# Kernel tuning notes

Measured on AMD Instinct MI355X. Metric: run time of the kernel, lower is better.

## Reference

```python
import jax, jax.numpy as jnp
import numpy as np
from jax import lax

DT = 0.1
B, T, SD, CD, H = 1024, 200, 64, 32, 512


def setup_inputs() -> dict:
    key = jax.random.key(0)
    k0, k1, k2, k3 = jax.random.split(key, 4)
    scale1 = 1.0 / np.sqrt(SD + CD)
    scale2 = 1.0 / np.sqrt(H)
    return {
        "x0": jax.random.normal(k0, (B, SD), dtype=jnp.float32),
        "controls": jax.random.normal(k1, (B, T, CD), dtype=jnp.float32),
        "W1": jax.random.normal(k2, (SD + CD, H), dtype=jnp.float32) * scale1,
        "b1": jnp.zeros((H,), dtype=jnp.float32),
        "W2": jax.random.normal(k3, (H, SD), dtype=jnp.float32) * scale2,
        "b2": jnp.zeros((SD,), dtype=jnp.float32),
    }


def reference(x0, controls, W1, b1, W2, b2):
    # dynamics: x_{t+1} = x + dt * MLP(concat(x, u)); rollout with true data dependency
    def step(x, u):
        h = jnp.tanh(jnp.concatenate([x, u], axis=-1) @ W1 + b1)  # [B, H]
        x_next = x + DT * (h @ W2 + b2)                           # [B, SD]
        return x_next, x_next

    controls_t = jnp.swapaxes(controls, 0, 1)  # [T, B, CD]
    _, xs = lax.scan(step, x0, controls_t)     # xs: [T, B, SD]
    states = jnp.concatenate([x0[:, None, :], jnp.swapaxes(xs, 0, 1)], axis=1)  # [B, T+1, SD]
    return states
```

## Files before the change

kernel.cpp:

```cpp
#include <hip/hip_runtime.h>
#include <cstddef>


constexpr int B_  = 1024;
constexpr int T_  = 200;
constexpr int SD_ = 64;
constexpr int CD_ = 32;
constexpr int H_  = 512;
constexpr int KD_ = SD_ + CD_;
constexpr float DT_ = 0.1f;
constexpr int ROWS_ = 4;
constexpr int THREADS_ = 1024;
constexpr int KHALF_ = 48;
constexpr int CHUNK_ = 32;

__global__ __launch_bounds__(THREADS_)
void rollout_split_kernel(
    const float* __restrict__ x0,
    const float* __restrict__ ctrl,
    const float* __restrict__ W1,
    const float* __restrict__ b1,
    const float* __restrict__ W2,
    const float* __restrict__ b2,
    float* __restrict__ out)
{
    __shared__ float xcT[KD_][ROWS_];
    __shared__ float part1[ROWS_][H_];
    __shared__ float hbuf[ROWS_][H_];
    __shared__ float part2[ROWS_][16][SD_];

    const int tid = threadIdx.x;
    const int r0  = blockIdx.x * ROWS_;

    const int j     = tid & (H_ - 1);
    const int g     = tid >> 9;
    const int kbase = g * KHALF_;
    float w1p[KHALF_];
    #pragma unroll
    for (int i = 0; i < KHALF_; ++i)
        w1p[i] = W1[(size_t)(kbase + i) * H_ + j];

    const int wv = tid >> 6;
    const int sl = tid & 63;
    const int jb = wv * CHUNK_;
    float w2p[CHUNK_];
    #pragma unroll
    for (int i = 0; i < CHUNK_; ++i)
        w2p[i] = W2[(size_t)(jb + i) * SD_ + sl];

    const float bj = b1[j];

    const int rf = (tid >> 6) & 3;
    const int sf = tid & 63;
    const float bs = b2[sf];

    const int  lt = tid - 512;
    const bool loader = (lt >= 0) && (lt < ROWS_ * CD_);
    const int  lr = (lt >> 5) & 3;
    const int  lc = lt & 31;
    const size_t ctrl_base = (size_t)(r0 + lr) * T_ * CD_ + lc;

    if (tid < ROWS_ * SD_) {
        const float v = x0[(size_t)(r0 + rf) * SD_ + sf];
        xcT[sf][rf] = v;
        out[(size_t)(r0 + rf) * (T_ + 1) * SD_ + sf] = v;
    }
    if (loader) xcT[SD_ + lc][lr] = ctrl[ctrl_base];
    __syncthreads();

    for (int t = 0; t < T_; ++t) {
        float cpre = 0.f;
        if (loader && (t + 1 < T_))
            cpre = ctrl[ctrl_base + (size_t)(t + 1) * CD_];

        float a0 = 0.f, a1 = 0.f, a2 = 0.f, a3 = 0.f;
        #pragma unroll
        for (int i = 0; i < KHALF_; ++i) {
            const float4 xv = *(const float4*)&xcT[kbase + i][0];
            const float  w  = w1p[i];
            a0 += xv.x * w;
            a1 += xv.y * w;
            a2 += xv.z * w;
            a3 += xv.w * w;
        }
        if (g == 1) {
            part1[0][j] = a0;  part1[1][j] = a1;
            part1[2][j] = a2;  part1[3][j] = a3;
        }
        __syncthreads();

        if (g == 0) {
            hbuf[0][j] = tanhf(bj + a0 + part1[0][j]);
            hbuf[1][j] = tanhf(bj + a1 + part1[1][j]);
            hbuf[2][j] = tanhf(bj + a2 + part1[2][j]);
            hbuf[3][j] = tanhf(bj + a3 + part1[3][j]);
        } else if (loader && (t + 1 < T_)) {
            xcT[SD_ + lc][lr] = cpre;
        }
        __syncthreads();

        #pragma unroll
        for (int r = 0; r < ROWS_; ++r) {
            float p = 0.f;
            #pragma unroll
            for (int i4 = 0; i4 < CHUNK_; i4 += 4) {
                const float4 hv = *(const float4*)&hbuf[r][jb + i4];
                p += hv.x * w2p[i4]     + hv.y * w2p[i4 + 1]
                   + hv.z * w2p[i4 + 2] + hv.w * w2p[i4 + 3];
            }
            part2[r][wv][sl] = p;
        }
        __syncthreads();

        if (tid < ROWS_ * SD_) {
            float acc = part2[rf][0][sf];
            #pragma unroll
            for (int c = 1; c < 16; ++c) acc += part2[rf][c][sf];
            const float xnew = xcT[sf][rf] + DT_ * (acc + bs);
            xcT[sf][rf] = xnew;
            out[(size_t)(r0 + rf) * (T_ + 1) * SD_ + (size_t)(t + 1) * SD_ + sf] = xnew;
        }
        __syncthreads();
    }
}

extern "C" void kernel_launch(void* const* d_in, const int* in_sizes, int n_in,
                              void* d_out, int out_size, void* d_ws, size_t ws_size,
                              hipStream_t stream) {
    const float* x0   = (const float*)d_in[0];
    const float* ctrl = (const float*)d_in[1];
    const float* W1   = (const float*)d_in[2];
    const float* b1   = (const float*)d_in[3];
    const float* W2   = (const float*)d_in[4];
    const float* b2   = (const float*)d_in[5];
    float* out = (float*)d_out;

    dim3 grid(B_ / ROWS_);
    dim3 block(THREADS_);
    rollout_split_kernel<<<grid, block, 0, stream>>>(x0, ctrl, W1, b1, W2, b2, out);
}
```

Before: 790.5 us.

## Split W1 reduction into four K-slices with packed float2 FMAs

Restructures the first matmul so each thread owns two hidden columns over a quarter of the K dimension, using packed two-wide FMA builtins. A shared-memory reduction over the four slices is then done by all 1024 threads, each computing two tanh values, so every thread does equal work instead of half the block idling during the tanh phase. The second matmul is also rewritten with packed FMAs over all four rows at once. The cost is a larger partial-sum buffer and more shared-memory traffic per step.

```diff
diff --git a/kernel.cpp b/kernel.cpp
--- a/kernel.cpp
+++ b/kernel.cpp
@@ -11,11 +11,14 @@
 constexpr float DT_ = 0.1f;
 constexpr int ROWS_ = 4;
 constexpr int THREADS_ = 1024;
-constexpr int KHALF_ = 48;
+constexpr int KSLICES_ = 4;
+constexpr int KLEN_ = KD_ / KSLICES_;
 constexpr int CHUNK_ = 32;
 
+typedef float f2 __attribute__((ext_vector_type(2)));
+
 __global__ __launch_bounds__(THREADS_)
-void rollout_split_kernel(
+void rollout_r12_kernel(
     const float* __restrict__ x0,
     const float* __restrict__ ctrl,
     const float* __restrict__ W1,
@@ -25,20 +28,21 @@
     float* __restrict__ out)
 {
     __shared__ float xcT[KD_][ROWS_];
-    __shared__ float part1[ROWS_][H_];
-    __shared__ float hbuf[ROWS_][H_];
+    __shared__ float part1[KSLICES_][ROWS_][H_];
+    __shared__ float pbuf[ROWS_][H_];
     __shared__ float part2[ROWS_][16][SD_];
 
     const int tid = threadIdx.x;
     const int r0  = blockIdx.x * ROWS_;
 
-    const int j     = tid & (H_ - 1);
-    const int g     = tid >> 9;
-    const int kbase = g * KHALF_;
-    float w1p[KHALF_];
+    const int jp    = tid & 255;
+    const int ks    = tid >> 8;
+    const int j0    = jp * 2;
+    const int kbase = ks * KLEN_;
+    f2 w1p[KLEN_];
     #pragma unroll
-    for (int i = 0; i < KHALF_; ++i)
-        w1p[i] = W1[(size_t)(kbase + i) * H_ + j];
+    for (int i = 0; i < KLEN_; ++i)
+        w1p[i] = *(const f2*)&W1[(size_t)(kbase + i) * H_ + j0];
 
     const int wv = tid >> 6;
     const int sl = tid & 63;
@@ -48,7 +52,9 @@
     for (int i = 0; i < CHUNK_; ++i)
         w2p[i] = W2[(size_t)(jb + i) * SD_ + sl];
 
-    const float bj = b1[j];
+    const int rF  = tid >> 8;
+    const int jjF = (tid & 255) * 2;
+    const f2 bj2 = {b1[jjF], b1[jjF + 1]};
 
     const int rf = (tid >> 6) & 3;
     const int sf = tid & 63;
@@ -73,42 +79,60 @@
         if (loader && (t + 1 < T_))
             cpre = ctrl[ctrl_base + (size_t)(t + 1) * CD_];
 
-        float a0 = 0.f, a1 = 0.f, a2 = 0.f, a3 = 0.f;
+        f2 a0 = {0.f, 0.f}, a1 = {0.f, 0.f}, a2 = {0.f, 0.f}, a3 = {0.f, 0.f};
         #pragma unroll
-        for (int i = 0; i < KHALF_; ++i) {
+        for (int i = 0; i < KLEN_; ++i) {
             const float4 xv = *(const float4*)&xcT[kbase + i][0];
-            const float  w  = w1p[i];
-            a0 += xv.x * w;
-            a1 += xv.y * w;
-            a2 += xv.z * w;
-            a3 += xv.w * w;
+            const f2 w = w1p[i];
+            a0 = __builtin_elementwise_fma(w, (f2){xv.x, xv.x}, a0);
+            a1 = __builtin_elementwise_fma(w, (f2){xv.y, xv.y}, a1);
+            a2 = __builtin_elementwise_fma(w, (f2){xv.z, xv.z}, a2);
+            a3 = __builtin_elementwise_fma(w, (f2){xv.w, xv.w}, a3);
         }
-        if (g == 1) {
-            part1[0][j] = a0;  part1[1][j] = a1;
-            part1[2][j] = a2;  part1[3][j] = a3;
+        *(f2*)&part1[ks][0][j0] = a0;
+        *(f2*)&part1[ks][1][j0] = a1;
+        *(f2*)&part1[ks][2][j0] = a2;
+        *(f2*)&part1[ks][3][j0] = a3;
+        __syncthreads();
+
+        {
+            f2 s = *(const f2*)&part1[0][rF][jjF];
+            s += *(const f2*)&part1[1][rF][jjF];
+            s += *(const f2*)&part1[2][rF][jjF];
+            s += *(const f2*)&part1[3][rF][jjF];
+            s += bj2;
+            f2 hv;
+            hv.x = tanhf(s.x);
+            hv.y = tanhf(s.y);
+            *(f2*)&pbuf[rF][jjF] = hv;
+            if (loader && (t + 1 < T_))
+                xcT[SD_ + lc][lr] = cpre;
         }
         __syncthreads();
 
-        if (g == 0) {
-            hbuf[0][j] = tanhf(bj + a0 + part1[0][j]);
-            hbuf[1][j] = tanhf(bj + a1 + part1[1][j]);
-            hbuf[2][j] = tanhf(bj + a2 + part1[2][j]);
-            hbuf[3][j] = tanhf(bj + a3 + part1[3][j]);
-        } else if (loader && (t + 1 < T_)) {
-            xcT[SD_ + lc][lr] = cpre;
-        }
-        __syncthreads();
-
-        #pragma unroll
-        for (int r = 0; r < ROWS_; ++r) {
-            float p = 0.f;
+        {
+            f2 q0 = {0.f, 0.f}, q1 = {0.f, 0.f}, q2 = {0.f, 0.f}, q3 = {0.f, 0.f};
             #pragma unroll
             for (int i4 = 0; i4 < CHUNK_; i4 += 4) {
-                const float4 hv = *(const float4*)&hbuf[r][jb + i4];
-                p += hv.x * w2p[i4]     + hv.y * w2p[i4 + 1]
-                   + hv.z * w2p[i4 + 2] + hv.w * w2p[i4 + 3];
+                const f2 wab = {w2p[i4 + 0], w2p[i4 + 1]};
+                const f2 wcd = {w2p[i4 + 2], w2p[i4 + 3]};
+                const float4 h0 = *(const float4*)&pbuf[0][jb + i4];
+                const float4 h1 = *(const float4*)&pbuf[1][jb + i4];
+                const float4 h2 = *(const float4*)&pbuf[2][jb + i4];
+                const float4 h3 = *(const float4*)&pbuf[3][jb + i4];
+                q0 = __builtin_elementwise_fma((f2){h0.x, h0.y}, wab, q0);
+                q0 = __builtin_elementwise_fma((f2){h0.z, h0.w}, wcd, q0);
+                q1 = __builtin_elementwise_fma((f2){h1.x, h1.y}, wab, q1);
+                q1 = __builtin_elementwise_fma((f2){h1.z, h1.w}, wcd, q1);
+                q2 = __builtin_elementwise_fma((f2){h2.x, h2.y}, wab, q2);
+                q2 = __builtin_elementwise_fma((f2){h2.z, h2.w}, wcd, q2);
+                q3 = __builtin_elementwise_fma((f2){h3.x, h3.y}, wab, q3);
+                q3 = __builtin_elementwise_fma((f2){h3.z, h3.w}, wcd, q3);
             }
-            part2[r][wv][sl] = p;
+            part2[0][wv][sl] = q0.x + q0.y;
+            part2[1][wv][sl] = q1.x + q1.y;
+            part2[2][wv][sl] = q2.x + q2.y;
+            part2[3][wv][sl] = q3.x + q3.y;
         }
         __syncthreads();
 
@@ -137,5 +161,5 @@
 
     dim3 grid(B_ / ROWS_);
     dim3 block(THREADS_);
-    rollout_split_kernel<<<grid, block, 0, stream>>>(x0, ctrl, W1, b1, W2, b2, out);
+    rollout_r12_kernel<<<grid, block, 0, stream>>>(x0, ctrl, W1, b1, W2, b2, out);
 }
```

Measured after the change: 707.0 us. -10.6%, faster.
